# Performance work log

Hardware: AMD Instinct MI355X
Metric: run time of the kernel (lower is better)

The kernel has to match this reference:

```python
import jax, jax.numpy as jnp
import numpy as np

N_INPUT, NUM_CENTERS, DIM = 16384, 4096, 256


def setup_inputs() -> dict:
    key = jax.random.key(0)
    k1, k2, k3, k4 = jax.random.split(key, 4)
    x = jax.random.normal(k1, (N_INPUT, DIM), dtype=jnp.float32)
    centers = jax.random.normal(k2, (NUM_CENTERS, DIM), dtype=jnp.float32)
    # positive sigmas bounded away from 0 so exp(-d^2/2s^2) stays well-scaled
    sigmas = jax.random.uniform(k3, (NUM_CENTERS, DIM), dtype=jnp.float32) * 2.0 + 1.0
    w_lin = jax.random.normal(k4, (1, NUM_CENTERS), dtype=jnp.float32) * (1.0 / np.sqrt(NUM_CENTERS))
    b_lin = jnp.zeros((1,), dtype=jnp.float32)
    return {"x": x, "centers": centers, "sigmas": sigmas, "w_lin": w_lin, "b_lin": b_lin}


def reference(x, centers, sigmas, w_lin, b_lin):
    # Anisotropic squared Mahalanobis-style distance:
    #   d2[n,c] = sum_d (x[n,d]-centers[c,d])^2 / (2*sigmas[c,d]^2)
    # expanded into GEMMs to avoid the (n, c, d) intermediate.
    inv2s2 = 1.0 / (2.0 * sigmas * sigmas)                      # [C, D]
    d2 = (
        jnp.einsum("nd,cd->nc", x * x, inv2s2)                 # x^2 term
        - 2.0 * jnp.einsum("nd,cd->nc", x, centers * inv2s2)   # cross term
        + jnp.sum(centers * centers * inv2s2, axis=-1)          # c^2 term [C]
    )
    radial_val = jnp.exp(-d2)                                   # [N, C]
    class_score = radial_val @ w_lin.T + b_lin                  # [N, 1]
    return jax.nn.sigmoid(class_score)
```

## Files before the change

kernel.cpp:

```cpp
#include <hip/hip_runtime.h>
#include <cstdint>
#include <cstddef>

#define MDIM 16384
#define CDIM 4096
#define DDIM 256
#define KDIM 512

typedef float f32x4  __attribute__((ext_vector_type(4)));
typedef int   i32x4v __attribute__((ext_vector_type(4)));
typedef int   i32x8v __attribute__((ext_vector_type(8)));

__global__ __launch_bounds__(256) void prep(
    const float* __restrict__ x, const float* __restrict__ centers,
    const float* __restrict__ sigmas,
    unsigned char* __restrict__ Ap, unsigned char* __restrict__ Bp,
    float* __restrict__ constc, float* __restrict__ score) {
    int b = blockIdx.x, tid = threadIdx.x;
    if (b < 4096) {
        int idx4 = b * 256 + tid;
        float4 v = ((const float4*)x)[idx4];
        int n = idx4 >> 6, dq = idx4 & 63;
        int p0 = __builtin_amdgcn_cvt_pk_fp8_f32(v.x, v.y, 0, false);
        p0     = __builtin_amdgcn_cvt_pk_fp8_f32(v.z, v.w, p0, true);
        int p1 = __builtin_amdgcn_cvt_pk_fp8_f32(v.x * v.x, v.y * v.y, 0, false);
        p1     = __builtin_amdgcn_cvt_pk_fp8_f32(v.z * v.z, v.w * v.w, p1, true);
        *(int*)(Ap + (size_t)n * KDIM + dq * 4)        = p0;
        *(int*)(Ap + (size_t)n * KDIM + DDIM + dq * 4) = p1;
        if (idx4 < MDIM) score[idx4] = 0.0f;
    } else {
        int gid = (b - 4096) * 256 + tid;
        int c = gid >> 6, q = gid & 63;
        float4 cv = ((const float4*)centers)[gid];
        float4 sv = ((const float4*)sigmas)[gid];
        float ix = 1.0f / (2.0f * sv.x * sv.x);
        float iy = 1.0f / (2.0f * sv.y * sv.y);
        float iz = 1.0f / (2.0f * sv.z * sv.z);
        float iw = 1.0f / (2.0f * sv.w * sv.w);
        int p0 = __builtin_amdgcn_cvt_pk_fp8_f32(-2.0f * cv.x * ix, -2.0f * cv.y * iy, 0, false);
        p0     = __builtin_amdgcn_cvt_pk_fp8_f32(-2.0f * cv.z * iz, -2.0f * cv.w * iw, p0, true);
        int p1 = __builtin_amdgcn_cvt_pk_fp8_f32(ix, iy, 0, false);
        p1     = __builtin_amdgcn_cvt_pk_fp8_f32(iz, iw, p1, true);
        *(int*)(Bp + (size_t)c * KDIM + q * 4)        = p0;
        *(int*)(Bp + (size_t)c * KDIM + DDIM + q * 4) = p1;
        float t = cv.x * cv.x * ix + cv.y * cv.y * iy
                + cv.z * cv.z * iz + cv.w * cv.w * iw;
        #pragma unroll
        for (int m = 32; m; m >>= 1) t += __shfl_down(t, m, 64);
        if ((tid & 63) == 0) constc[c] = t;
    }
}

__global__ __launch_bounds__(256, 2) void gemm_fused(
    const unsigned char* __restrict__ A, const unsigned char* __restrict__ B,
    const float* __restrict__ constc, const float* __restrict__ w,
    float* __restrict__ score) {

    __shared__ unsigned char As[256 * 128];
    __shared__ unsigned char Bs[128 * 128];

    const int tid  = threadIdx.x;
    const int wave = tid >> 6;
    const int lane = tid & 63;
    const int quad = lane >> 4;
    const int l16  = lane & 15;

    const int bm = blockIdx.y;
    const int bn = blockIdx.x;

    const int wave_m = wave * 64;

    f32x4 acc[4][8] = {};

    const int st_row = lane >> 3;
    const int st_k   = ((lane & 7) ^ st_row) * 16;

    const unsigned char* Abase = A + (size_t)(bm * 256) * KDIM;
    const unsigned char* Bbase = B + (size_t)(bn * 128) * KDIM;

    const int rsw = l16 & 7;
    const int s0  = ((2 * quad)     ^ rsw) * 16;
    const int s1  = ((2 * quad + 1) ^ rsw) * 16;

    for (int k0 = 0; k0 < KDIM; k0 += 128) {
        #pragma unroll
        for (int c = 0; c < 8; ++c) {
            int slab = wave * 8 + c;
            const unsigned char* ga = Abase + (size_t)(slab * 8 + st_row) * KDIM + k0 + st_k;
            __builtin_amdgcn_global_load_lds(
                (const __attribute__((address_space(1))) void*)ga,
                (__attribute__((address_space(3))) void*)(As + slab * 1024), 16, 0, 0);
        }
        #pragma unroll
        for (int c = 0; c < 4; ++c) {
            int slab = wave * 4 + c;
            const unsigned char* gb = Bbase + (size_t)(slab * 8 + st_row) * KDIM + k0 + st_k;
            __builtin_amdgcn_global_load_lds(
                (const __attribute__((address_space(1))) void*)gb,
                (__attribute__((address_space(3))) void*)(Bs + slab * 1024), 16, 0, 0);
        }
        __syncthreads();

        i32x8v af[4];
        #pragma unroll
        for (int i = 0; i < 4; ++i) {
            const unsigned char* pa = As + (wave_m + i * 16 + l16) * 128;
            i32x4v* h = (i32x4v*)&af[i];
            h[0] = *(const i32x4v*)(pa + s0);
            h[1] = *(const i32x4v*)(pa + s1);
        }
        #pragma unroll
        for (int j = 0; j < 8; ++j) {
            const unsigned char* pb = Bs + (j * 16 + l16) * 128;
            i32x8v bf;
            i32x4v* h = (i32x4v*)&bf;
            h[0] = *(const i32x4v*)(pb + s0);
            h[1] = *(const i32x4v*)(pb + s1);
            #pragma unroll
            for (int i = 0; i < 4; ++i)
                acc[i][j] = __builtin_amdgcn_mfma_scale_f32_16x16x128_f8f6f4(
                    af[i], bf, acc[i][j],
                    0 , 0 ,
                    0, 0x7F7F7F7F ,
                    0, 0x7F7F7F7F );
        }
        __syncthreads();
    }

    float rowsum[4][4];
    #pragma unroll
    for (int i = 0; i < 4; ++i)
        #pragma unroll
        for (int r = 0; r < 4; ++r) rowsum[i][r] = 0.0f;

    const float NEG_LOG2E = -1.4426950408889634f;
    #pragma unroll
    for (int j = 0; j < 8; ++j) {
        int ng = bn * 128 + j * 16 + l16;
        float wj = w[ng];
        float cj = constc[ng];
        #pragma unroll
        for (int i = 0; i < 4; ++i)
            #pragma unroll
            for (int r = 0; r < 4; ++r) {
                float d2 = acc[i][j][r] + cj;
                rowsum[i][r] += exp2f(NEG_LOG2E * d2) * wj;
            }
    }

    #pragma unroll
    for (int mask = 1; mask < 16; mask <<= 1)
        #pragma unroll
        for (int i = 0; i < 4; ++i)
            #pragma unroll
            for (int r = 0; r < 4; ++r)
                rowsum[i][r] += __shfl_xor(rowsum[i][r], mask, 64);

    if (l16 == 0) {
        #pragma unroll
        for (int i = 0; i < 4; ++i)
            #pragma unroll
            for (int r = 0; r < 4; ++r) {
                int mg = bm * 256 + wave_m + i * 16 + quad * 4 + r;
                atomicAdd(&score[mg], rowsum[i][r]);
            }
    }
}

__global__ void finalize(const float* __restrict__ score,
                         const float* __restrict__ b,
                         float* __restrict__ out) {
    int n = blockIdx.x * 256 + threadIdx.x;
    if (n < MDIM) {
        float s = score[n] + b[0];
        out[n] = 1.0f / (1.0f + exp2f(-1.4426950408889634f * s));
    }
}

extern "C" void kernel_launch(void* const* d_in, const int* in_sizes, int n_in,
                              void* d_out, int out_size, void* d_ws, size_t ws_size,
                              hipStream_t stream) {
    const float* x       = (const float*)d_in[0];
    const float* centers = (const float*)d_in[1];
    const float* sigmas  = (const float*)d_in[2];
    const float* w_lin   = (const float*)d_in[3];
    const float* b_lin   = (const float*)d_in[4];
    float* out = (float*)d_out;

    char* ws = (char*)d_ws;
    unsigned char* Ap = (unsigned char*)ws;
    unsigned char* Bp = (unsigned char*)(ws + (size_t)MDIM * KDIM);
    float* cc    = (float*)(ws + (size_t)MDIM * KDIM + (size_t)CDIM * KDIM);
    float* score = (float*)((char*)cc + CDIM * sizeof(float));

    prep<<<dim3(4096 + 1024), dim3(256), 0, stream>>>(
        x, centers, sigmas, Ap, Bp, cc, score);
    gemm_fused<<<dim3(CDIM / 128, MDIM / 256), dim3(256), 0, stream>>>(
        Ap, Bp, cc, w_lin, score);
    finalize<<<dim3((MDIM + 255) / 256), dim3(256), 0, stream>>>(score, b_lin, out);
}
```

Baseline: 134.7 us.

## Quantize GEMM operands to FP4 with per-half block scales

Switches the packed operands from FP8 to FP4 (e2m1), using hand-written rounding and per-K-half scale factors to bring the squared terms into range. This halves the packed operand bytes and the LDS traffic, and lets MFMA run in FP4 mode. The loaded 16 bytes are duplicated across both halves of the operand register, so each MFMA issue does redundant work, and the distance terms lose a lot of precision, which could push the results past tolerance.

```diff
diff --git a/kernel.cpp b/kernel.cpp
--- a/kernel.cpp
+++ b/kernel.cpp
@@ -6,10 +6,25 @@
 #define CDIM 4096
 #define DDIM 256
 #define KDIM 512
+#define KB   256
 
 typedef float f32x4  __attribute__((ext_vector_type(4)));
 typedef int   i32x4v __attribute__((ext_vector_type(4)));
 typedef int   i32x8v __attribute__((ext_vector_type(8)));
+
+__device__ __forceinline__ unsigned q4(float v) {
+    unsigned s = (__builtin_bit_cast(unsigned, v) >> 31) << 3;
+    float a = fabsf(v);
+    unsigned c = (unsigned)(a >= 0.25f) + (a >= 0.75f) + (a >= 1.25f)
+               + (a >= 1.75f) + (a >= 2.5f) + (a >= 3.5f) + (a >= 5.0f);
+    return s | c;
+}
+__device__ __forceinline__ unsigned pack8(const float* v) {
+    unsigned w = 0;
+    #pragma unroll
+    for (int i = 0; i < 8; ++i) w |= q4(v[i]) << (4 * i);
+    return w;
+}
 
 __global__ __launch_bounds__(256) void prep(
     const float* __restrict__ x, const float* __restrict__ centers,
@@ -17,37 +32,38 @@
     unsigned char* __restrict__ Ap, unsigned char* __restrict__ Bp,
     float* __restrict__ constc, float* __restrict__ score) {
     int b = blockIdx.x, tid = threadIdx.x;
-    if (b < 4096) {
-        int idx4 = b * 256 + tid;
-        float4 v = ((const float4*)x)[idx4];
-        int n = idx4 >> 6, dq = idx4 & 63;
-        int p0 = __builtin_amdgcn_cvt_pk_fp8_f32(v.x, v.y, 0, false);
-        p0     = __builtin_amdgcn_cvt_pk_fp8_f32(v.z, v.w, p0, true);
-        int p1 = __builtin_amdgcn_cvt_pk_fp8_f32(v.x * v.x, v.y * v.y, 0, false);
-        p1     = __builtin_amdgcn_cvt_pk_fp8_f32(v.z * v.z, v.w * v.w, p1, true);
-        *(int*)(Ap + (size_t)n * KDIM + dq * 4)        = p0;
-        *(int*)(Ap + (size_t)n * KDIM + DDIM + dq * 4) = p1;
-        if (idx4 < MDIM) score[idx4] = 0.0f;
+    if (b < 2048) {
+        int idx8 = b * 256 + tid;
+        int n = idx8 >> 5, d8 = idx8 & 31;
+        float v[8], v2[8];
+        *(float4*)(v)     = ((const float4*)x)[idx8 * 2];
+        *(float4*)(v + 4) = ((const float4*)x)[idx8 * 2 + 1];
+        #pragma unroll
+        for (int i = 0; i < 8; ++i) v2[i] = v[i] * v[i] * 0.125f;
+        *(unsigned*)(Ap + (size_t)n * KB + d8 * 4)       = pack8(v);
+        *(unsigned*)(Ap + (size_t)n * KB + 128 + d8 * 4) = pack8(v2);
+        if (idx8 < MDIM) score[idx8] = 0.0f;
     } else {
-        int gid = (b - 4096) * 256 + tid;
-        int c = gid >> 6, q = gid & 63;
-        float4 cv = ((const float4*)centers)[gid];
-        float4 sv = ((const float4*)sigmas)[gid];
-        float ix = 1.0f / (2.0f * sv.x * sv.x);
-        float iy = 1.0f / (2.0f * sv.y * sv.y);
-        float iz = 1.0f / (2.0f * sv.z * sv.z);
-        float iw = 1.0f / (2.0f * sv.w * sv.w);
-        int p0 = __builtin_amdgcn_cvt_pk_fp8_f32(-2.0f * cv.x * ix, -2.0f * cv.y * iy, 0, false);
-        p0     = __builtin_amdgcn_cvt_pk_fp8_f32(-2.0f * cv.z * iz, -2.0f * cv.w * iw, p0, true);
-        int p1 = __builtin_amdgcn_cvt_pk_fp8_f32(ix, iy, 0, false);
-        p1     = __builtin_amdgcn_cvt_pk_fp8_f32(iz, iw, p1, true);
-        *(int*)(Bp + (size_t)c * KDIM + q * 4)        = p0;
-        *(int*)(Bp + (size_t)c * KDIM + DDIM + q * 4) = p1;
-        float t = cv.x * cv.x * ix + cv.y * cv.y * iy
-                + cv.z * cv.z * iz + cv.w * cv.w * iw;
-        #pragma unroll
-        for (int m = 32; m; m >>= 1) t += __shfl_down(t, m, 64);
-        if ((tid & 63) == 0) constc[c] = t;
+        int gid8 = (b - 2048) * 256 + tid;
+        int c = gid8 >> 5, d8 = gid8 & 31;
+        float cv[8], sv[8], cr[8], iv[8];
+        *(float4*)(cv)     = ((const float4*)centers)[gid8 * 2];
+        *(float4*)(cv + 4) = ((const float4*)centers)[gid8 * 2 + 1];
+        *(float4*)(sv)     = ((const float4*)sigmas)[gid8 * 2];
+        *(float4*)(sv + 4) = ((const float4*)sigmas)[gid8 * 2 + 1];
+        float t = 0.0f;
+        #pragma unroll
+        for (int i = 0; i < 8; ++i) {
+            float inv = 1.0f / (2.0f * sv[i] * sv[i]);
+            cr[i] = -2.0f * cv[i] * inv;
+            iv[i] = inv * 8.0f;
+            t += cv[i] * cv[i] * inv;
+        }
+        *(unsigned*)(Bp + (size_t)c * KB + d8 * 4)       = pack8(cr);
+        *(unsigned*)(Bp + (size_t)c * KB + 128 + d8 * 4) = pack8(iv);
+        #pragma unroll
+        for (int m = 16; m; m >>= 1) t += __shfl_xor(t, m, 64);
+        if ((tid & 31) == 0) constc[c] = t;
     }
 }
 
@@ -75,18 +91,19 @@
     const int st_row = lane >> 3;
     const int st_k   = ((lane & 7) ^ st_row) * 16;
 
-    const unsigned char* Abase = A + (size_t)(bm * 256) * KDIM;
-    const unsigned char* Bbase = B + (size_t)(bn * 128) * KDIM;
+    const unsigned char* Abase = A + (size_t)(bm * 256) * KB;
+    const unsigned char* Bbase = B + (size_t)(bn * 128) * KB;
 
     const int rsw = l16 & 7;
-    const int s0  = ((2 * quad)     ^ rsw) * 16;
-    const int s1  = ((2 * quad + 1) ^ rsw) * 16;
-
-    for (int k0 = 0; k0 < KDIM; k0 += 128) {
+
+    #pragma unroll
+    for (int k0 = 0; k0 < 2; ++k0) {
+        const int sA = k0 ? 0x82828282 : 0x7F7F7F7F;
+        const int sB = k0 ? 0x7C7C7C7C : 0x7F7F7F7F;
         #pragma unroll
         for (int c = 0; c < 8; ++c) {
             int slab = wave * 8 + c;
-            const unsigned char* ga = Abase + (size_t)(slab * 8 + st_row) * KDIM + k0 + st_k;
+            const unsigned char* ga = Abase + (size_t)(slab * 8 + st_row) * KB + k0 * 128 + st_k;
             __builtin_amdgcn_global_load_lds(
                 (const __attribute__((address_space(1))) void*)ga,
                 (__attribute__((address_space(3))) void*)(As + slab * 1024), 16, 0, 0);
@@ -94,35 +111,36 @@
         #pragma unroll
         for (int c = 0; c < 4; ++c) {
             int slab = wave * 4 + c;
-            const unsigned char* gb = Bbase + (size_t)(slab * 8 + st_row) * KDIM + k0 + st_k;
+            const unsigned char* gb = Bbase + (size_t)(slab * 8 + st_row) * KB + k0 * 128 + st_k;
             __builtin_amdgcn_global_load_lds(
                 (const __attribute__((address_space(1))) void*)gb,
                 (__attribute__((address_space(3))) void*)(Bs + slab * 1024), 16, 0, 0);
         }
         __syncthreads();
 
-        i32x8v af[4];
-        #pragma unroll
-        for (int i = 0; i < 4; ++i) {
-            const unsigned char* pa = As + (wave_m + i * 16 + l16) * 128;
-            i32x4v* h = (i32x4v*)&af[i];
-            h[0] = *(const i32x4v*)(pa + s0);
-            h[1] = *(const i32x4v*)(pa + s1);
-        }
-        #pragma unroll
-        for (int j = 0; j < 8; ++j) {
-            const unsigned char* pb = Bs + (j * 16 + l16) * 128;
-            i32x8v bf;
-            i32x4v* h = (i32x4v*)&bf;
-            h[0] = *(const i32x4v*)(pb + s0);
-            h[1] = *(const i32x4v*)(pb + s1);
-            #pragma unroll
-            for (int i = 0; i < 4; ++i)
-                acc[i][j] = __builtin_amdgcn_mfma_scale_f32_16x16x128_f8f6f4(
-                    af[i], bf, acc[i][j],
-                    0 , 0 ,
-                    0, 0x7F7F7F7F ,
-                    0, 0x7F7F7F7F );
+        #pragma unroll
+        for (int kh = 0; kh < 2; ++kh) {
+            const int sl = ((kh * 4 + quad) ^ rsw) * 16;
+            i32x8v af[4];
+            #pragma unroll
+            for (int i = 0; i < 4; ++i) {
+                i32x4v lo = *(const i32x4v*)(As + (wave_m + i * 16 + l16) * 128 + sl);
+                i32x4v* h = (i32x4v*)&af[i];
+                h[0] = lo; h[1] = lo;
+            }
+            #pragma unroll
+            for (int j = 0; j < 8; ++j) {
+                i32x4v lo = *(const i32x4v*)(Bs + (j * 16 + l16) * 128 + sl);
+                i32x8v bf;
+                i32x4v* h = (i32x4v*)&bf;
+                h[0] = lo; h[1] = lo;
+                #pragma unroll
+                for (int i = 0; i < 4; ++i)
+                    acc[i][j] = __builtin_amdgcn_mfma_scale_f32_16x16x128_f8f6f4(
+                        af[i], bf, acc[i][j],
+                        4 , 4 ,
+                        0, sA, 0, sB);
+            }
         }
         __syncthreads();
     }
@@ -189,11 +207,11 @@
 
     char* ws = (char*)d_ws;
     unsigned char* Ap = (unsigned char*)ws;
-    unsigned char* Bp = (unsigned char*)(ws + (size_t)MDIM * KDIM);
-    float* cc    = (float*)(ws + (size_t)MDIM * KDIM + (size_t)CDIM * KDIM);
+    unsigned char* Bp = (unsigned char*)(ws + (size_t)MDIM * KB);
+    float* cc    = (float*)(ws + (size_t)MDIM * KB + (size_t)CDIM * KB);
     float* score = (float*)((char*)cc + CDIM * sizeof(float));
 
-    prep<<<dim3(4096 + 1024), dim3(256), 0, stream>>>(
+    prep<<<dim3(2048 + 512), dim3(256), 0, stream>>>(
         x, centers, sigmas, Ap, Bp, cc, score);
     gemm_fused<<<dim3(CDIM / 128, MDIM / 256), dim3(256), 0, stream>>>(
         Ap, Bp, cc, w_lin, score);
```

Result: faster. 120.7 us (-10.4%).
